# Optimization experiments

Measured on AMD Instinct MI355X. Metric: run time of the kernel, lower is better.

The kernel has to match this reference:

```python
import jax, jax.numpy as jnp
import numpy as np

HEADS = 16
NEG = -1e9  # matches masked_fill(-1000000000.0)

def setup_inputs() -> dict:
    key = jax.random.key(0)
    ks = jax.random.split(key, 7)
    B, T, C = 2, 2048, 1024
    s = 1.0 / np.sqrt(C)
    return {
        "q": jax.random.normal(ks[0], (B, T, C), jnp.float32),
        "k": jax.random.normal(ks[1], (B, T, C), jnp.float32),
        "v": jax.random.normal(ks[2], (B, T, C), jnp.float32),
        "Wq": jax.random.normal(ks[3], (C, C), jnp.float32) * s,
        "Wk": jax.random.normal(ks[4], (C, C), jnp.float32) * s,
        "Wv": jax.random.normal(ks[5], (C, C), jnp.float32) * s,
        "Wo": jax.random.normal(ks[6], (C, C), jnp.float32) * s,
    }

def reference(q, k, v, Wq, Wk, Wv, Wo):
    B, T, C = q.shape
    h = HEADS
    dk = C // h
    # torch Linear (no bias): y = x @ W.T ; weight is [out, in]
    def proj(x, W):
        return (x @ W.T).reshape(B, T, h, dk).transpose(0, 2, 1, 3)  # [B,h,T,dk]
    qh, kh, vh = proj(q, Wq), proj(k, Wk), proj(v, Wv)
    scale = jnp.asarray(dk, q.dtype) ** 0.5
    scores = jnp.einsum('bhqd,bhkd->bhqk', qh / scale, kh)  # [B,h,T,T]
    causal = jnp.tril(jnp.ones((T, T), dtype=bool))
    scores = jnp.where(causal[None, None], scores, jnp.asarray(NEG, scores.dtype))
    attn = jax.nn.softmax(scores, axis=-1)
    out = jnp.einsum('bhqk,bhkd->bhqd', attn, vh)  # [B,h,T,dk]
    concat = out.transpose(0, 2, 1, 3).reshape(B, T, C)
    return concat @ Wo.T
```

## Files before the change

kernel.cpp:

```cpp
#include <hip/hip_runtime.h>
#include <hip/hip_bf16.h>

typedef __bf16 bf16x8 __attribute__((ext_vector_type(8)));
typedef float  f32x4  __attribute__((ext_vector_type(4)));
typedef unsigned short u16;

__device__ __forceinline__ u16 f2bf(float f) {
    __bf16 h = (__bf16)f;
    return __builtin_bit_cast(u16, h);
}

__device__ __forceinline__ f32x4 mfma16(bf16x8 a, bf16x8 b, f32x4 c) {
    return __builtin_amdgcn_mfma_f32_16x16x32_bf16(a, b, c, 0, 0, 0);
}

__device__ __forceinline__ bf16x8 cvt8(float4 a0, float4 a1) {
    bf16x8 u;
    u[0] = (__bf16)a0.x; u[1] = (__bf16)a0.y; u[2] = (__bf16)a0.z; u[3] = (__bf16)a0.w;
    u[4] = (__bf16)a1.x; u[5] = (__bf16)a1.y; u[6] = (__bf16)a1.z; u[7] = (__bf16)a1.w;
    return u;
}

__global__ __launch_bounds__(256) void cvtW(const float* __restrict__ W0,
                                            const float* __restrict__ W1,
                                            const float* __restrict__ W2,
                                            const float* __restrict__ W3,
                                            u16* __restrict__ dst) {
    const int t     = blockIdx.x * 256 + threadIdx.x;
    const int which = t >> 17;
    const int off   = (t & 0x1FFFF) * 8;
    const float* s  = (which == 0) ? W0 : (which == 1) ? W1 : (which == 2) ? W2 : W3;
    float4 f0 = *(const float4*)(s + off);
    float4 f1 = *(const float4*)(s + off + 4);
    *(bf16x8*)(dst + ((size_t)which << 20) + off) = cvt8(f0, f1);
}

__global__ __launch_bounds__(512, 4) void gemm_qkv(const float* __restrict__ q,
                                                   const float* __restrict__ k,
                                                   const float* __restrict__ v,
                                                   const u16* __restrict__ Wb,
                                                   u16* __restrict__ Qp,
                                                   u16* __restrict__ Kp,
                                                   u16* __restrict__ Vt) {
    constexpr int K = 1024, N = 1024;
    __shared__ __align__(16) u16 As[128 * 32];
    __shared__ __align__(16) u16 Bs[256 * 32];

    const int tid  = threadIdx.x;
    const int lane = tid & 63;
    const int w    = tid >> 6;
    const int wr = w >> 2, wc = w & 3;
    const int wg    = (blockIdx.x & 7) * 48 + (blockIdx.x >> 3);
    const int which = wg >> 7;
    const int inner = wg & 127;
    const int m0 = (inner >> 2) * 128, n0 = (inner & 3) * 256;
    const int colg = lane & 15, rowg = lane >> 4;

    const float* A = (which == 0) ? q : (which == 1) ? k : v;
    const u16*   W = Wb + ((size_t)which << 20);

    const int rowA = tid >> 2, kcA = tid & 3;
    const size_t aoff = (size_t)(m0 + rowA) * K + kcA * 8;
    const int wiA = rowA * 32 + (kcA ^ ((rowA >> 1) & 3)) * 8;

    size_t boff[2];
    int wiB[2];
#pragma unroll
    for (int i = 0; i < 2; ++i) {
        const int c   = i * 512 + tid;
        const int row = c >> 2;
        const int kc  = c & 3;
        boff[i] = (size_t)(n0 + row) * K + kc * 8;
        wiB[i] = row * 32 + (kc ^ ((row >> 1) & 3)) * 8;
    }

    const int kcr   = rowg ^ ((colg >> 1) & 3);
    const int rbase = colg * 32 + kcr * 8;

    f32x4 acc[4][4];
#pragma unroll
    for (int i = 0; i < 4; ++i)
#pragma unroll
        for (int j = 0; j < 4; ++j) acc[i][j] = (f32x4){0.f, 0.f, 0.f, 0.f};

    for (int t = 0; t < 32; ++t) {
        const int kk = t * 32;
        float4 a0 = *(const float4*)(A + aoff + kk);
        float4 a1 = *(const float4*)(A + aoff + kk + 4);
        uint4  bv0 = *(const uint4*)(W + boff[0] + kk);
        uint4  bv1 = *(const uint4*)(W + boff[1] + kk);
        *(bf16x8*)(&As[wiA]) = cvt8(a0, a1);
        *(uint4*)(&Bs[wiB[0]]) = bv0;
        *(uint4*)(&Bs[wiB[1]]) = bv1;
        __syncthreads();

        bf16x8 af[4], bfr[4];
#pragma unroll
        for (int mi = 0; mi < 4; ++mi)
            af[mi] = *(const bf16x8*)(&As[(wr * 64 + mi * 16) * 32 + rbase]);
#pragma unroll
        for (int ni = 0; ni < 4; ++ni)
            bfr[ni] = *(const bf16x8*)(&Bs[(wc * 64 + ni * 16) * 32 + rbase]);
#pragma unroll
        for (int mi = 0; mi < 4; ++mi)
#pragma unroll
            for (int ni = 0; ni < 4; ++ni)
                acc[mi][ni] = mfma16(af[mi], bfr[ni], acc[mi][ni]);
        __syncthreads();
    }

    u16* Crm = (which == 0) ? Qp : Kp;
#pragma unroll
    for (int mi = 0; mi < 4; ++mi) {
#pragma unroll
        for (int ni = 0; ni < 4; ++ni) {
#pragma unroll
            for (int r = 0; r < 4; ++r) {
                const int row = m0 + wr * 64 + mi * 16 + rowg * 4 + r;
                const int col = n0 + wc * 64 + ni * 16 + colg;
                const float vv = acc[mi][ni][r];
                if (which < 2) {
                    Crm[(size_t)row * N + col] = f2bf(vv);
                } else {
                    const int b = row >> 11, tt = row & 2047;
                    const int h = col >> 6,  d = col & 63;
                    Vt[((size_t)((b * 16 + h) * 64 + d) << 11) + tt] = f2bf(vv);
                }
            }
        }
    }
}

__global__ __launch_bounds__(256) void gemm_out(const u16* __restrict__ Ap,
                                                const u16* __restrict__ W,
                                                float* __restrict__ Cp) {
    constexpr int K = 1024, N = 1024;
    __shared__ __align__(16) u16 As[2][2048];
    __shared__ __align__(16) u16 Bs[2][4096];

    const int tid  = threadIdx.x;
    const int lane = tid & 63;
    const int w    = tid >> 6;
    const int wr = w >> 1, wc = w & 1;
    const int wg = (blockIdx.x & 7) * 64 + (blockIdx.x >> 3);
    const int m0 = (wg >> 3) * 64, n0 = (wg & 7) * 128;
    const int colg = lane & 15, rowg = lane >> 4;

    const int rowA = tid >> 2, kcA = tid & 3;
    const size_t aoff = (size_t)(m0 + rowA) * K + kcA * 8;
    const int wiA = rowA * 32 + (kcA ^ ((rowA >> 1) & 3)) * 8;

    size_t boff[2];
    int wiB[2];
#pragma unroll
    for (int i = 0; i < 2; ++i) {
        const int c   = i * 256 + tid;
        const int row = c >> 2;
        const int kc  = c & 3;
        boff[i] = (size_t)(n0 + row) * K + kc * 8;
        wiB[i] = row * 32 + (kc ^ ((row >> 1) & 3)) * 8;
    }
    const int kcr   = rowg ^ ((colg >> 1) & 3);
    const int rbase = colg * 32 + kcr * 8;

    f32x4 acc[2][4];
#pragma unroll
    for (int i = 0; i < 2; ++i)
#pragma unroll
        for (int j = 0; j < 4; ++j) acc[i][j] = (f32x4){0.f, 0.f, 0.f, 0.f};

    uint4 av = *(const uint4*)(Ap + aoff);
    uint4 bv[2];
#pragma unroll
    for (int i = 0; i < 2; ++i) bv[i] = *(const uint4*)(W + boff[i]);
    *(uint4*)(&As[0][wiA]) = av;
#pragma unroll
    for (int i = 0; i < 2; ++i) *(uint4*)(&Bs[0][wiB[i]]) = bv[i];
    __syncthreads();

    int p = 0;
    for (int t = 0; t < 32; ++t) {
        if (t < 31) {
            const int kk = (t + 1) * 32;
            av = *(const uint4*)(Ap + aoff + kk);
#pragma unroll
            for (int i = 0; i < 2; ++i) bv[i] = *(const uint4*)(W + boff[i] + kk);
        }
        {
            bf16x8 af[2], bfr[4];
#pragma unroll
            for (int mi = 0; mi < 2; ++mi)
                af[mi] = *(const bf16x8*)(&As[p][(wr * 32 + mi * 16) * 32 + rbase]);
#pragma unroll
            for (int ni = 0; ni < 4; ++ni)
                bfr[ni] = *(const bf16x8*)(&Bs[p][(wc * 64 + ni * 16) * 32 + rbase]);
#pragma unroll
            for (int mi = 0; mi < 2; ++mi)
#pragma unroll
                for (int ni = 0; ni < 4; ++ni)
                    acc[mi][ni] = mfma16(af[mi], bfr[ni], acc[mi][ni]);
        }
        if (t < 31) {
            *(uint4*)(&As[p ^ 1][wiA]) = av;
#pragma unroll
            for (int i = 0; i < 2; ++i) *(uint4*)(&Bs[p ^ 1][wiB[i]]) = bv[i];
        }
        __syncthreads();
        p ^= 1;
    }

#pragma unroll
    for (int mi = 0; mi < 2; ++mi)
#pragma unroll
        for (int ni = 0; ni < 4; ++ni)
#pragma unroll
            for (int r = 0; r < 4; ++r) {
                const int row = m0 + wr * 32 + mi * 16 + rowg * 4 + r;
                const int col = n0 + wc * 64 + ni * 16 + colg;
                Cp[(size_t)row * N + col] = acc[mi][ni][r];
            }
}

constexpr float CEXP = 0.18033688011112042f;

__global__ __launch_bounds__(256) void attn_causal(const u16* __restrict__ Qp,
                                                   const u16* __restrict__ Kp,
                                                   const u16* __restrict__ Vt,
                                                   u16* __restrict__ concat) {
    constexpr int T = 2048, C = 1024;
    __shared__ __align__(16) u16 Ks[128 * 64];
    __shared__ __align__(16) u16 Vs[64 * 128];
    __shared__ __align__(16) u16 Pl[4][2048];

    const int tid  = threadIdx.x;
    const int lane = tid & 63;
    const int w    = tid >> 6;
    const int colg = lane & 15, rowg = lane >> 4;

    const int idx = blockIdx.x;
    const int xcd = idx & 7;
    const int i1  = idx >> 3;
    const int bh  = xcd * 4 + (i1 & 3);
    const int qg  = 31 - (i1 >> 2);
    const int b = bh >> 4, h = bh & 15;

    const int q0 = (qg * 4 + w) * 16;
    const int nt    = (q0 + 143) >> 7;
    const int ktmax = ((qg * 4 + 3) * 16 + 143) >> 7;

    const char* Kg = (const char*)(Kp + (size_t)(b * T) * C + h * 64);
    const char* Vg = (const char*)(Vt + ((size_t)(b * 16 + h) * 64) * T);
    char* Ksb = (char*)Ks;
    char* Vsb = (char*)Vs;
    char* Pw  = (char*)&Pl[w][0];

    const u16* Qb = Qp + (size_t)(b * T + q0 + colg) * C + h * 64;
    const bf16x8 qf0 = *(const bf16x8*)(Qb + rowg * 8);
    const bf16x8 qf1 = *(const bf16x8*)(Qb + 32 + rowg * 8);

    float mm = -1e30f, ll = 0.f;
    f32x4 O[4];
#pragma unroll
    for (int g = 0; g < 4; ++g) O[g] = (f32x4){0.f, 0.f, 0.f, 0.f};

    const int sw = (colg & 7) << 4;

    for (int kt = 0; kt < ktmax; ++kt) {
        const int kvb = kt * 128;
        uint4 kst[4], vst[4];
#pragma unroll
        for (int i2 = 0; i2 < 4; ++i2) {
            const int s  = i2 * 4096 + tid * 16;
            const int kv = s >> 7, ir = s & 127;
            kst[i2] = *(const uint4*)(Kg + (size_t)(kvb + kv) * 2048 + ir);
            const int d = s >> 8, irv = s & 255;
            vst[i2] = *(const uint4*)(Vg + (size_t)d * 4096 + (size_t)kvb * 2 + irv);
        }
#pragma unroll
        for (int i2 = 0; i2 < 4; ++i2) {
            const int s  = i2 * 4096 + tid * 16;
            const int kv = s >> 7;
            *(uint4*)(Ksb + (s ^ ((kv & 7) << 4))) = kst[i2];
            const int d = s >> 8;
            *(uint4*)(Vsb + (s ^ ((d & 7) << 4))) = vst[i2];
        }
        __syncthreads();

        if (kt < nt) {
            float pr[8][4];
#pragma unroll
            for (int sub = 0; sub < 8; ++sub) {
                const int kb = (sub * 16 + colg) * 128 + rowg * 16;
                bf16x8 kf0 = *(const bf16x8*)(Ksb + (kb ^ sw));
                bf16x8 kf1 = *(const bf16x8*)(Ksb + ((kb + 64) ^ sw));
                f32x4 t = (f32x4){0.f, 0.f, 0.f, 0.f};
                t = mfma16(kf0, qf0, t);
                t = mfma16(kf1, qf1, t);
#pragma unroll
                for (int r = 0; r < 4; ++r) pr[sub][r] = t[r];
            }
            if (kvb + 127 > q0) {
#pragma unroll
                for (int sub = 0; sub < 8; ++sub)
#pragma unroll
                    for (int r = 0; r < 4; ++r)
                        if (kvb + sub * 16 + rowg * 4 + r > q0 + colg) pr[sub][r] = -1e30f;
            }
            float mx[8];
#pragma unroll
            for (int sub = 0; sub < 8; ++sub)
                mx[sub] = fmaxf(fmaxf(pr[sub][0], pr[sub][1]), fmaxf(pr[sub][2], pr[sub][3]));
            float pm = fmaxf(fmaxf(fmaxf(mx[0], mx[1]), fmaxf(mx[2], mx[3])),
                             fmaxf(fmaxf(mx[4], mx[5]), fmaxf(mx[6], mx[7])));
            pm = fmaxf(pm, __shfl_xor(pm, 16, 64));
            pm = fmaxf(pm, __shfl_xor(pm, 32, 64));
            if (__any(pm > mm + 40.f)) {
                const float mn = fmaxf(mm, pm);
                const float sc = __builtin_amdgcn_exp2f((mm - mn) * CEXP);
                mm = mn;
                ll *= sc;
#pragma unroll
                for (int r = 0; r < 4; ++r) {
                    const float scr = __shfl(sc, (lane & 48) + rowg * 4 + r, 64);
#pragma unroll
                    for (int g = 0; g < 4; ++g) O[g][r] *= scr;
                }
            }
            float rs = 0.f;
#pragma unroll
            for (int sub = 0; sub < 8; ++sub) {
                const float e0 = __builtin_amdgcn_exp2f((pr[sub][0] - mm) * CEXP);
                const float e1 = __builtin_amdgcn_exp2f((pr[sub][1] - mm) * CEXP);
                const float e2 = __builtin_amdgcn_exp2f((pr[sub][2] - mm) * CEXP);
                const float e3 = __builtin_amdgcn_exp2f((pr[sub][3] - mm) * CEXP);
                pr[sub][0] = e0; pr[sub][1] = e1; pr[sub][2] = e2; pr[sub][3] = e3;
                rs += (e0 + e1) + (e2 + e3);
            }
            rs += __shfl_xor(rs, 16, 64);
            rs += __shfl_xor(rs, 32, 64);
            ll += rs;
#pragma unroll
            for (int sub = 0; sub < 8; ++sub) {
                uint2 pk;
                pk.x = (unsigned)f2bf(pr[sub][0]) | ((unsigned)f2bf(pr[sub][1]) << 16);
                pk.y = (unsigned)f2bf(pr[sub][2]) | ((unsigned)f2bf(pr[sub][3]) << 16);
                const int wb = (colg * 256 + sub * 32 + rowg * 8) ^ sw;
                *(uint2*)(Pw + wb) = pk;
            }
            bf16x8 pf[4];
#pragma unroll
            for (int kc = 0; kc < 4; ++kc)
                pf[kc] = *(const bf16x8*)(Pw + ((colg * 256 + kc * 64 + rowg * 16) ^ sw));
#pragma unroll
            for (int g = 0; g < 4; ++g) {
                const int vb0 = (g * 16 + colg) * 256 + rowg * 16;
#pragma unroll
                for (int kc = 0; kc < 4; ++kc) {
                    bf16x8 vf = *(const bf16x8*)(Vsb + ((vb0 + kc * 64) ^ sw));
                    O[g] = mfma16(pf[kc], vf, O[g]);
                }
            }
        }
        __syncthreads();
    }

#pragma unroll
    for (int r = 0; r < 4; ++r) {
        const float lr = __shfl(ll, (lane & 48) + rowg * 4 + r, 64);
        const float rc = 1.f / lr;
        const size_t base = (size_t)(b * T + q0 + rowg * 4 + r) * C + h * 64;
#pragma unroll
        for (int g = 0; g < 4; ++g)
            concat[base + g * 16 + colg] = f2bf(O[g][r] * rc);
    }
}

extern "C" void kernel_launch(void* const* d_in, const int* in_sizes, int n_in,
                              void* d_out, int out_size, void* d_ws, size_t ws_size,
                              hipStream_t stream) {
    const float* q  = (const float*)d_in[0];
    const float* k  = (const float*)d_in[1];
    const float* v  = (const float*)d_in[2];
    const float* Wq = (const float*)d_in[3];
    const float* Wk = (const float*)d_in[4];
    const float* Wv = (const float*)d_in[5];
    const float* Wo = (const float*)d_in[6];
    float* out = (float*)d_out;

    constexpr size_t NELEM = (size_t)4096 * 1024;
    constexpr size_t WSZ   = (size_t)1 << 20;
    u16* Wbf = (u16*)d_ws;
    u16* Qp  = Wbf + 4 * WSZ;
    u16* Kp  = Qp + NELEM;
    u16* Vt  = Kp + NELEM;
    u16* Cc  = Vt + NELEM;

    cvtW<<<2048, 256, 0, stream>>>(Wq, Wk, Wv, Wo, Wbf);

    gemm_qkv<<<384, 512, 0, stream>>>(q, k, v, Wbf, Qp, Kp, Vt);

    attn_causal<<<1024, 256, 0, stream>>>(Qp, Kp, Vt, Cc);

    gemm_out<<<512, 256, 0, stream>>>(Cc, Wbf + 3 * WSZ, out);
}
```

Measured before the change: 139.0 us.

## Pre-convert activations to bf16 and double-buffer QKV GEMM via global_load_lds

```diff
diff --git a/kernel.cpp b/kernel.cpp
--- a/kernel.cpp
+++ b/kernel.cpp
@@ -21,102 +21,126 @@
     return u;
 }
 
-__global__ __launch_bounds__(256) void cvtW(const float* __restrict__ W0,
-                                            const float* __restrict__ W1,
-                                            const float* __restrict__ W2,
-                                            const float* __restrict__ W3,
+__device__ __forceinline__ void gload16(const u16* g, u16* l) {
+    __builtin_amdgcn_global_load_lds(
+        (const __attribute__((address_space(1))) void*)g,
+        (__attribute__((address_space(3))) void*)l, 16, 0, 0);
+}
+
+__global__ __launch_bounds__(256) void cvt7(const float* __restrict__ q,
+                                            const float* __restrict__ k,
+                                            const float* __restrict__ v,
+                                            const float* __restrict__ Wq,
+                                            const float* __restrict__ Wk,
+                                            const float* __restrict__ Wv,
+                                            const float* __restrict__ Wo,
                                             u16* __restrict__ dst) {
-    const int t     = blockIdx.x * 256 + threadIdx.x;
-    const int which = t >> 17;
-    const int off   = (t & 0x1FFFF) * 8;
-    const float* s  = (which == 0) ? W0 : (which == 1) ? W1 : (which == 2) ? W2 : W3;
+    const int t = blockIdx.x * 256 + threadIdx.x;
+    const float* s;
+    int o;
+    if (t < 0x80000)       { s = q; o = t; }
+    else if (t < 0x100000) { s = k; o = t - 0x80000; }
+    else if (t < 0x180000) { s = v; o = t - 0x100000; }
+    else {
+        const int r = t - 0x180000;
+        const int w = r >> 17;
+        o = r & 0x1FFFF;
+        s = (w == 0) ? Wq : (w == 1) ? Wk : (w == 2) ? Wv : Wo;
+    }
+    const int off = o * 8;
     float4 f0 = *(const float4*)(s + off);
     float4 f1 = *(const float4*)(s + off + 4);
-    *(bf16x8*)(dst + ((size_t)which << 20) + off) = cvt8(f0, f1);
-}
-
-__global__ __launch_bounds__(512, 4) void gemm_qkv(const float* __restrict__ q,
-                                                   const float* __restrict__ k,
-                                                   const float* __restrict__ v,
+    *(bf16x8*)(dst + (size_t)t * 8) = cvt8(f0, f1);
+}
+
+__global__ __launch_bounds__(512, 2) void gemm_qkv(const u16* __restrict__ qb,
+                                                   const u16* __restrict__ kb,
+                                                   const u16* __restrict__ vb,
                                                    const u16* __restrict__ Wb,
                                                    u16* __restrict__ Qp,
                                                    u16* __restrict__ Kp,
                                                    u16* __restrict__ Vt) {
     constexpr int K = 1024, N = 1024;
-    __shared__ __align__(16) u16 As[128 * 32];
-    __shared__ __align__(16) u16 Bs[256 * 32];
+    __shared__ __align__(16) u16 As[2][256 * 64];
+    __shared__ __align__(16) u16 Bs[2][256 * 64];
 
     const int tid  = threadIdx.x;
     const int lane = tid & 63;
     const int w    = tid >> 6;
     const int wr = w >> 2, wc = w & 3;
-    const int wg    = (blockIdx.x & 7) * 48 + (blockIdx.x >> 3);
-    const int which = wg >> 7;
-    const int inner = wg & 127;
-    const int m0 = (inner >> 2) * 128, n0 = (inner & 3) * 256;
+    const int wg    = (blockIdx.x & 7) * 24 + (blockIdx.x >> 3);
+    const int which = wg >> 6;
+    const int inner = wg & 63;
+    const int m0 = (inner >> 2) * 256, n0 = (inner & 3) * 256;
     const int colg = lane & 15, rowg = lane >> 4;
 
-    const float* A = (which == 0) ? q : (which == 1) ? k : v;
-    const u16*   W = Wb + ((size_t)which << 20);
-
-    const int rowA = tid >> 2, kcA = tid & 3;
-    const size_t aoff = (size_t)(m0 + rowA) * K + kcA * 8;
-    const int wiA = rowA * 32 + (kcA ^ ((rowA >> 1) & 3)) * 8;
-
-    size_t boff[2];
-    int wiB[2];
-#pragma unroll
-    for (int i = 0; i < 2; ++i) {
+    const u16* A = (which == 0) ? qb : (which == 1) ? kb : vb;
+    const u16* W = Wb + ((size_t)which << 20);
+
+    size_t soff[4];
+    int dofs[4];
+#pragma unroll
+    for (int i = 0; i < 4; ++i) {
         const int c   = i * 512 + tid;
-        const int row = c >> 2;
-        const int kc  = c & 3;
-        boff[i] = (size_t)(n0 + row) * K + kc * 8;
-        wiB[i] = row * 32 + (kc ^ ((row >> 1) & 3)) * 8;
-    }
-
-    const int kcr   = rowg ^ ((colg >> 1) & 3);
-    const int rbase = colg * 32 + kcr * 8;
-
-    f32x4 acc[4][4];
-#pragma unroll
-    for (int i = 0; i < 4; ++i)
+        const int row = c >> 3;
+        const int co  = c & 7;
+        soff[i] = (size_t)row * K + co * 8;
+        dofs[i] = c * 8;
+    }
+
+    f32x4 acc[8][4];
+#pragma unroll
+    for (int i = 0; i < 8; ++i)
 #pragma unroll
         for (int j = 0; j < 4; ++j) acc[i][j] = (f32x4){0.f, 0.f, 0.f, 0.f};
 
-    for (int t = 0; t < 32; ++t) {
-        const int kk = t * 32;
-        float4 a0 = *(const float4*)(A + aoff + kk);
-        float4 a1 = *(const float4*)(A + aoff + kk + 4);
-        uint4  bv0 = *(const uint4*)(W + boff[0] + kk);
-        uint4  bv1 = *(const uint4*)(W + boff[1] + kk);
-        *(bf16x8*)(&As[wiA]) = cvt8(a0, a1);
-        *(uint4*)(&Bs[wiB[0]]) = bv0;
-        *(uint4*)(&Bs[wiB[1]]) = bv1;
+    const u16* Abase = A + (size_t)m0 * K;
+    const u16* Bbase = W + (size_t)n0 * K;
+
+#pragma unroll
+    for (int i = 0; i < 4; ++i) {
+        gload16(Abase + soff[i], &As[0][dofs[i]]);
+        gload16(Bbase + soff[i], &Bs[0][dofs[i]]);
+    }
+    __syncthreads();
+
+    int p = 0;
+    for (int t = 0; t < 16; ++t) {
+        if (t < 15) {
+            const int kk = (t + 1) * 64;
+#pragma unroll
+            for (int i = 0; i < 4; ++i) {
+                gload16(Abase + soff[i] + kk, &As[p ^ 1][dofs[i]]);
+                gload16(Bbase + soff[i] + kk, &Bs[p ^ 1][dofs[i]]);
+            }
+        }
+#pragma unroll
+        for (int ks = 0; ks < 2; ++ks) {
+            bf16x8 af[8], bfr[4];
+#pragma unroll
+            for (int mi = 0; mi < 8; ++mi)
+                af[mi] = *(const bf16x8*)(&As[p][(wr * 128 + mi * 16 + colg) * 64 + ks * 32 + rowg * 8]);
+#pragma unroll
+            for (int ni = 0; ni < 4; ++ni)
+                bfr[ni] = *(const bf16x8*)(&Bs[p][(wc * 64 + ni * 16 + colg) * 64 + ks * 32 + rowg * 8]);
+#pragma unroll
+            for (int mi = 0; mi < 8; ++mi)
+#pragma unroll
+                for (int ni = 0; ni < 4; ++ni)
+                    acc[mi][ni] = mfma16(af[mi], bfr[ni], acc[mi][ni]);
+        }
         __syncthreads();
-
-        bf16x8 af[4], bfr[4];
-#pragma unroll
-        for (int mi = 0; mi < 4; ++mi)
-            af[mi] = *(const bf16x8*)(&As[(wr * 64 + mi * 16) * 32 + rbase]);
-#pragma unroll
-        for (int ni = 0; ni < 4; ++ni)
-            bfr[ni] = *(const bf16x8*)(&Bs[(wc * 64 + ni * 16) * 32 + rbase]);
-#pragma unroll
-        for (int mi = 0; mi < 4; ++mi)
-#pragma unroll
-            for (int ni = 0; ni < 4; ++ni)
-                acc[mi][ni] = mfma16(af[mi], bfr[ni], acc[mi][ni]);
-        __syncthreads();
+        p ^= 1;
     }
 
     u16* Crm = (which == 0) ? Qp : Kp;
 #pragma unroll
-    for (int mi = 0; mi < 4; ++mi) {
+    for (int mi = 0; mi < 8; ++mi) {
 #pragma unroll
         for (int ni = 0; ni < 4; ++ni) {
 #pragma unroll
             for (int r = 0; r < 4; ++r) {
-                const int row = m0 + wr * 64 + mi * 16 + rowg * 4 + r;
+                const int row = m0 + wr * 128 + mi * 16 + rowg * 4 + r;
                 const int col = n0 + wc * 64 + ni * 16 + colg;
                 const float vv = acc[mi][ni][r];
                 if (which < 2) {
@@ -389,15 +413,18 @@
 
     constexpr size_t NELEM = (size_t)4096 * 1024;
     constexpr size_t WSZ   = (size_t)1 << 20;
-    u16* Wbf = (u16*)d_ws;
+    u16* QB  = (u16*)d_ws;
+    u16* KB  = QB + NELEM;
+    u16* VB  = KB + NELEM;
+    u16* Wbf = VB + NELEM;
     u16* Qp  = Wbf + 4 * WSZ;
     u16* Kp  = Qp + NELEM;
     u16* Vt  = Kp + NELEM;
     u16* Cc  = Vt + NELEM;
 
-    cvtW<<<2048, 256, 0, stream>>>(Wq, Wk, Wv, Wo, Wbf);
-
-    gemm_qkv<<<384, 512, 0, stream>>>(q, k, v, Wbf, Qp, Kp, Vt);
+    cvt7<<<8192, 256, 0, stream>>>(q, k, v, Wq, Wk, Wv, Wo, QB);
+
+    gemm_qkv<<<192, 512, 0, stream>>>(QB, KB, VB, Wbf, Qp, Kp, Vt);
 
     attn_causal<<<1024, 256, 0, stream>>>(Qp, Kp, Vt, Cc);
 
```

Measured after the change: 154.4 us. 11.1% more time.
